# Performance work log

Hardware: AMD Instinct MI355X
Metric: run time of the kernel (lower is better)

The kernel has to match this reference:

```python
import jax, jax.numpy as jnp
import numpy as np
import math

B, S, D, K = 8, 2048, 1024, 64
EPS = 1e-5

def _ln(x):
    m = jnp.mean(x, axis=-1, keepdims=True)
    v = jnp.mean((x - m) ** 2, axis=-1, keepdims=True)
    return (x - m) * jax.lax.rsqrt(v + EPS)

def setup_inputs() -> dict:
    key = jax.random.key(0)
    ks = jax.random.split(key, 14)
    s = 0.02
    return {
        "x":  jax.random.normal(ks[0], (B, S, D), dtype=jnp.float32),
        "Wk": jax.random.normal(ks[1], (D, K), dtype=jnp.float32) * s,
        "bk": jnp.zeros((K,), dtype=jnp.float32),
        "Wq": jax.random.normal(ks[2], (D, K), dtype=jnp.float32) * s,
        "bq": jnp.zeros((K,), dtype=jnp.float32),
        "Wv": jax.random.normal(ks[3], (D, D), dtype=jnp.float32) * s,
        "bv": jnp.zeros((D,), dtype=jnp.float32),
        "Wb": jax.random.normal(ks[4], (D, 1), dtype=jnp.float32) * s,
        "bb": jnp.zeros((1,), dtype=jnp.float32),
        "W1": jax.random.normal(ks[5], (D, D), dtype=jnp.float32) * s,
        "b1": jnp.zeros((D,), dtype=jnp.float32),
        "g1": jnp.ones((D,), dtype=jnp.float32),
        "be1": jnp.zeros((D,), dtype=jnp.float32),
    }

def reference(x, Wk, bk, Wq, bq, Wv, bv, Wb, bb, W1, b1, g1, be1):
    scale = 1.0 / math.sqrt(K)
    keys    = (jnp.einsum('bsd,dk->bsk', x, Wk) + bk) * scale   # [B,S,K]
    queries = jnp.einsum('bsd,dk->bsk', x, Wq) + bq             # [B,S,K]
    values  = jnp.einsum('bsd,de->bse', x, Wv) + bv             # [B,S,D]
    biases  = jnp.einsum('bsd,do->bso', x, Wb) + bb             # [B,S,1]
    # scores[b,i,j] = keys[b,i] . queries[b,j] + biases[b,i]
    scores = jax.nn.sigmoid(jnp.einsum('bik,bjk->bij', keys, queries) + biases)
    attention = jnp.einsum('bij,bjd->bid', scores, values)      # [B,S,D]
    res = _ln(x + attention) * g1 + be1
    feedforward = jax.nn.relu(jnp.einsum('bsd,de->bse', res, W1) + b1)
    return _ln(res + feedforward)
```

## Files before the change

### kernel.cpp

```cpp
#include <hip/hip_runtime.h>
#include <math.h>


typedef __bf16 bf16_t;
typedef __bf16 bf16x4_t __attribute__((ext_vector_type(4)));
typedef __bf16 bf16x8_t __attribute__((ext_vector_type(8)));
typedef float  f32x4    __attribute__((ext_vector_type(4)));

#define DEV static __device__ __forceinline__

DEV void gll16(const void* g, void* l) {
  __builtin_amdgcn_global_load_lds(
      (const __attribute__((address_space(1))) void*)g,
      (__attribute__((address_space(3))) void*)l, 16, 0, 0);
}

template <int MODE, int MFAST>
__global__ __launch_bounds__(512, 2) void gemm256p(
    const bf16_t* __restrict__ A, const bf16_t* __restrict__ B,
    bf16_t* __restrict__ C, int K, int lda, int ldb, int ldc,
    long sAb, long sBb, long sCb, const float* __restrict__ aux0) {
  const int gx = gridDim.x, gy = gridDim.y;
  const int gxy = gx * gy;
  const int nwg = gxy * (int)gridDim.z;
  const int orig = blockIdx.x + gx * blockIdx.y + gxy * blockIdx.z;
  const int lid = (orig & 7) * (nwg >> 3) + (orig >> 3);
  const int bz = lid / gxy;
  const int rem = lid - bz * gxy;
  const int bx = MFAST ? (rem / gy) : (rem % gx);
  const int by = MFAST ? (rem % gy) : (rem / gx);

  A += (long)bz * sAb;
  B += (long)bz * sBb;
  const int m0 = by * 256, n0 = bx * 256;

  __shared__ bf16_t SM[65536];
#define ASH(b, h) (&SM[(((b)*2 + (h)) << 13)])
#define BSH(b, h) (&SM[32768 + (((b)*2 + (h)) << 13)])

  const int tid = threadIdx.x;
  const int wid = tid >> 6, l = tid & 63;
  const int wr = wid >> 2, wc = wid & 3;
  const int lr = l & 15, lh = l >> 4;

  const int sRow = tid >> 2;
  const int sSl = (tid & 3) ^ ((tid >> 3) & 3);
  const bf16_t* Asrc = A + (long)(m0 + sRow) * lda + sSl * 8;
  const bf16_t* Bsrc = B + (long)(n0 + sRow) * ldb + sSl * 8;
  const long aStep = (long)128 * lda, bStep = (long)128 * ldb;

#define STAGE_A(b, h, kt) do { \
    const bf16_t* s_ = Asrc + (kt) * 64 + (h) * 32; \
    gll16(s_,         ASH(b, h) + tid * 8); \
    gll16(s_ + aStep, ASH(b, h) + 4096 + tid * 8); } while (0)
#define STAGE_B(b, h, kt) do { \
    const bf16_t* s_ = Bsrc + (kt) * 64 + (h) * 32; \
    gll16(s_,         BSH(b, h) + tid * 8); \
    gll16(s_ + bStep, BSH(b, h) + 4096 + tid * 8); } while (0)

  const int sw = (lh ^ ((lr >> 1) & 3)) * 8;
  const int aOff = (wr * 128 + lr) * 32 + sw;
  const int bOff = (wc * 64 + lr) * 32 + sw;

  f32x4 acc[8][4] = {};
  const int NT = K >> 6;

#define LGKM(n) do { \
    asm volatile("s_waitcnt lgkmcnt(" #n ")" ::: "memory"); \
    __builtin_amdgcn_sched_barrier(0); } while (0)
#define MFMA16(AS, BS, mo) do { \
    __builtin_amdgcn_s_setprio(1); \
    _Pragma("unroll") for (int m = 0; m < 4; ++m) \
    _Pragma("unroll") for (int n = 0; n < 4; ++n) \
      acc[m + (mo)][n] = __builtin_amdgcn_mfma_f32_16x16x32_bf16(AS[m], BS[n], acc[m + (mo)][n], 0, 0, 0); \
    __builtin_amdgcn_s_setprio(0); } while (0)

  STAGE_A(0, 0, 0); STAGE_B(0, 0, 0); STAGE_A(0, 1, 0); STAGE_B(0, 1, 0);
  asm volatile("s_waitcnt vmcnt(4)" ::: "memory");
  __builtin_amdgcn_s_barrier();

  bf16x8_t aA[4], aB[4], bA[4], bB[4];
#pragma unroll
  for (int n = 0; n < 4; ++n) bA[n] = *(const bf16x8_t*)(BSH(0, 0) + bOff + n * 512);
#pragma unroll
  for (int m = 0; m < 4; ++m) aA[m] = *(const bf16x8_t*)(ASH(0, 0) + aOff + m * 512);

  for (int t = 0; t < NT; ++t) {
    const int p = t & 1, q = p ^ 1;
    const bool pf = (t + 1 < NT);

#pragma unroll
    for (int m = 0; m < 4; ++m) aB[m] = *(const bf16x8_t*)(ASH(p, 0) + aOff + (m + 4) * 512);
    if (pf) STAGE_A(q, 0, t + 1);
    LGKM(4);
    MFMA16(aA, bA, 0);

    if (pf) {
      asm volatile("s_waitcnt vmcnt(2)" ::: "memory");
    } else {
      asm volatile("s_waitcnt vmcnt(0)" ::: "memory");
    }
    __builtin_amdgcn_sched_barrier(0);
    __builtin_amdgcn_s_barrier();
#pragma unroll
    for (int m = 0; m < 4; ++m) aA[m] = *(const bf16x8_t*)(ASH(p, 1) + aOff + m * 512);
#pragma unroll
    for (int n = 0; n < 4; ++n) bB[n] = *(const bf16x8_t*)(BSH(p, 1) + bOff + n * 512);
    if (pf) STAGE_B(q, 0, t + 1);
    LGKM(8);
    MFMA16(aB, bA, 4);

#pragma unroll
    for (int m = 0; m < 4; ++m) aB[m] = *(const bf16x8_t*)(ASH(p, 1) + aOff + (m + 4) * 512);
    if (pf) STAGE_A(q, 1, t + 1);
    LGKM(4);
    MFMA16(aA, bB, 0);

    if (pf) STAGE_B(q, 1, t + 1);
    asm volatile("s_waitcnt lgkmcnt(0)" ::: "memory");
    if (pf) {
      asm volatile("s_waitcnt vmcnt(4)" ::: "memory");
    }
    __builtin_amdgcn_sched_barrier(0);
    __builtin_amdgcn_s_barrier();
    if (pf) {
#pragma unroll
      for (int n = 0; n < 4; ++n) bA[n] = *(const bf16x8_t*)(BSH(q, 0) + bOff + n * 512);
#pragma unroll
      for (int m = 0; m < 4; ++m) aA[m] = *(const bf16x8_t*)(ASH(q, 0) + aOff + m * 512);
    }
    __builtin_amdgcn_sched_barrier(0);
    MFMA16(aB, bB, 4);
  }
#undef STAGE_A
#undef STAGE_B
#undef LGKM
#undef MFMA16

  bf16_t* Cb = C + (long)bz * sCb;
  const int rowb = m0 + wr * 128 + lh * 4;
  const int colb = n0 + wc * 64 + lr;
#pragma unroll
  for (int m = 0; m < 8; ++m)
#pragma unroll
    for (int n = 0; n < 4; ++n) {
      const f32x4 v = acc[m][n];
      const int cc = colb + n * 16;
#pragma unroll
      for (int r = 0; r < 4; ++r) {
        const int rr = rowb + m * 16 + r;
        const float val = v[r];
        if constexpr (MODE == 1) {
          Cb[(long)rr * ldc + cc] = (bf16_t)(val + aux0[rr]);
        } else if constexpr (MODE == 3) {
          Cb[(long)rr * ldc + cc] = (bf16_t)val;
        } else {
          Cb[(long)rr * ldc + cc] = (bf16_t)fmaxf(val + aux0[cc], 0.0f);
        }
      }
    }
#undef ASH
#undef BSH
}

__global__ __launch_bounds__(256) void scores128(
    const bf16_t* __restrict__ kq, bf16_t* __restrict__ C,
    const float* __restrict__ biases) {
  const int orig = blockIdx.x + 16 * blockIdx.y + 256 * blockIdx.z;
  const int lid = (orig & 7) * 256 + (orig >> 3);
  const int bz = lid >> 8;
  const int rem = lid & 255;
  const int bx = rem & 15, by = rem >> 4;

  const bf16_t* A = kq + (long)bz * 2048 * 128;
  const bf16_t* B = A + 64;
  const float* a0 = biases + (long)bz * 2048;
  const int m0 = by * 128, n0 = bx * 128;

  __shared__ bf16_t SM[16384];
#define ASH(h) (&SM[(h) << 12])
#define BSH(h) (&SM[8192 + ((h) << 12)])

  const int tid = threadIdx.x;
  const int w = tid >> 6, l = tid & 63;
  const int wr = w >> 1, wc = w & 1;
  const int lr = l & 15, lh = l >> 4;

  const int sRow = tid >> 2;
  const int sSl = ((tid & 3) ^ ((tid >> 3) & 3)) * 8;
  const bf16_t* As = A + (long)(m0 + sRow) * 128 + sSl;
  const bf16_t* Bs = B + (long)(n0 + sRow) * 128 + sSl;
#pragma unroll
  for (int h = 0; h < 2; ++h) {
    gll16(As + h * 32, ASH(h) + tid * 8);
    gll16(As + h * 32 + 64 * 128, ASH(h) + 2048 + tid * 8);
    gll16(Bs + h * 32, BSH(h) + tid * 8);
    gll16(Bs + h * 32 + 64 * 128, BSH(h) + 2048 + tid * 8);
  }
  asm volatile("s_waitcnt vmcnt(0)" ::: "memory");
  __builtin_amdgcn_s_barrier();

  const int sw = (lh ^ ((lr >> 1) & 3)) * 8;
  const int aOff = (wr * 64 + lr) * 32 + sw;
  const int bOff = (wc * 64 + lr) * 32 + sw;

  f32x4 acc[4][4] = {};
#pragma unroll
  for (int h = 0; h < 2; ++h) {
    bf16x8_t aF[4], bF[4];
#pragma unroll
    for (int m = 0; m < 4; ++m) aF[m] = *(const bf16x8_t*)(ASH(h) + aOff + m * 512);
#pragma unroll
    for (int n = 0; n < 4; ++n) bF[n] = *(const bf16x8_t*)(BSH(h) + bOff + n * 512);
#pragma unroll
    for (int m = 0; m < 4; ++m)
#pragma unroll
      for (int n = 0; n < 4; ++n)
        acc[m][n] = __builtin_amdgcn_mfma_f32_16x16x32_bf16(aF[m], bF[n], acc[m][n], 0, 0, 0);
  }

  __builtin_amdgcn_s_barrier();
  {
    const int rowb = (wr << 6) + (lh << 2);
    const int colb = (wc << 6) + lr;
#pragma unroll
    for (int m = 0; m < 4; ++m)
#pragma unroll
      for (int n = 0; n < 4; ++n) {
        const f32x4 v = acc[m][n];
        const int cl = colb + (n << 4);
#pragma unroll
        for (int r = 0; r < 4; ++r) {
          const int rl = rowb + (m << 4) + r;
          const float zz = v[r] + a0[m0 + rl];
          SM[rl * 128 + (cl ^ (lh << 4))] =
              (bf16_t)__builtin_amdgcn_rcpf(1.0f + __expf(-zz));
        }
      }
    __syncthreads();
    bf16_t* Cb = C + (long)bz * 2048 * 2048;
    const int chunk = tid & 15, rsub = tid >> 4;
#pragma unroll
    for (int pp = 0; pp < 8; ++pp) {
      const int rl = pp * 16 + rsub;
      const int sc = chunk ^ (((rl >> 2) & 3) << 1);
      const bf16x8_t vv = *(const bf16x8_t*)&SM[rl * 128 + sc * 8];
      *(bf16x8_t*)&Cb[(long)(m0 + rl) * 2048 + n0 + chunk * 8] = vv;
    }
  }
#undef ASH
#undef BSH
}

__global__ __launch_bounds__(256) void kq_thin(
    const bf16_t* __restrict__ A, const bf16_t* __restrict__ B,
    bf16_t* __restrict__ C,
    const float* __restrict__ bk, const float* __restrict__ bq) {
  const int m0 = blockIdx.x * 64;

  __shared__ bf16_t SM[12288];
#define ASH(b) (&SM[(b) << 11])
#define BSH(b) (&SM[4096 + ((b) << 12)])

  const int tid = threadIdx.x;
  const int w = tid >> 6, l = tid & 63;
  const int lr = l & 15, lh = l >> 4;

  const int sRow = tid >> 2;
  const int sSl = (tid & 3) ^ ((tid >> 3) & 3);
  const bf16_t* Asrc = A + (long)(m0 + sRow) * 1024 + sSl * 8;
  const bf16_t* Bsrc0 = B + (long)sRow * 1024 + sSl * 8;
  const bf16_t* Bsrc1 = B + (long)(64 + sRow) * 1024 + sSl * 8;

  const int sw = (lh ^ ((lr >> 1) & 3)) * 8;
  const int aOff = (w * 16 + lr) * 32 + sw;

  f32x4 acc[8] = {};

  auto stage = [&](int buf, int k0) {
    gll16(Asrc + k0, ASH(buf) + tid * 8);
    gll16(Bsrc0 + k0, BSH(buf) + tid * 8);
    gll16(Bsrc1 + k0, BSH(buf) + 2048 + tid * 8);
  };

  stage(0, 0);
  __syncthreads();
  int cur = 0;

  for (int k0 = 0; k0 < 1024; k0 += 32) {
    if (k0 + 32 < 1024) stage(cur ^ 1, k0 + 32);

    const bf16x8_t aF = *(const bf16x8_t*)(ASH(cur) + aOff);
    bf16x8_t bF[8];
#pragma unroll
    for (int j = 0; j < 8; ++j)
      bF[j] = *(const bf16x8_t*)(BSH(cur) + (j * 16 + lr) * 32 + sw);
#pragma unroll
    for (int j = 0; j < 8; ++j)
      acc[j] = __builtin_amdgcn_mfma_f32_16x16x32_bf16(aF, bF[j], acc[j], 0, 0, 0);

    __syncthreads();
    cur ^= 1;
  }

  {
#pragma unroll
    for (int j = 0; j < 8; ++j) {
      const f32x4 v = acc[j];
      const int cl = j * 16 + lr;
      const float b = (cl < 64) ? bk[cl] : bq[cl - 64];
      const float s = (cl < 64) ? 0.125f : 1.0f;
#pragma unroll
      for (int r = 0; r < 4; ++r) {
        const int rl = w * 16 + lh * 4 + r;
        SM[rl * 128 + (cl ^ (lh << 4))] = (bf16_t)((v[r] + b) * s);
      }
    }
    __syncthreads();
    const int chunk = tid & 15, rsub = tid >> 4;
#pragma unroll
    for (int pp = 0; pp < 4; ++pp) {
      const int rl = pp * 16 + rsub;
      const int sc = chunk ^ (((rl >> 2) & 3) << 1);
      const bf16x8_t vv = *(const bf16x8_t*)&SM[rl * 128 + sc * 8];
      *(bf16x8_t*)&C[(long)(m0 + rl) * 128 + chunk * 8] = vv;
    }
  }
#undef ASH
#undef BSH
}

__global__ __launch_bounds__(256) void cast_bias_kernel(
    const float* __restrict__ x, const float* __restrict__ Wb,
    const float* __restrict__ bb, bf16_t* __restrict__ x_bf,
    float* __restrict__ biases) {
  const int r = blockIdx.x * 4 + (threadIdx.x >> 6);
  const int l = threadIdx.x & 63;
  const float* xr = x + (long)r * 1024;
  bf16_t* orow = x_bf + (long)r * 1024;
  float s = 0.f;
#pragma unroll
  for (int i = 0; i < 4; ++i) {
    const int off = l * 4 + i * 256;
    const float4 v = *(const float4*)(xr + off);
    const float4 w = *(const float4*)(Wb + off);
    s += v.x * w.x + v.y * w.y + v.z * w.z + v.w * w.w;
    bf16x4_t o;
    o[0] = (bf16_t)v.x; o[1] = (bf16_t)v.y; o[2] = (bf16_t)v.z; o[3] = (bf16_t)v.w;
    *(bf16x4_t*)(orow + off) = o;
  }
#pragma unroll
  for (int off = 1; off < 64; off <<= 1) s += __shfl_xor(s, off);
  if (l == 0) biases[r] = s + bb[0];
}

__global__ __launch_bounds__(256) void transpose_cast_kernel(
    const float* __restrict__ in, bf16_t* __restrict__ out, int R, int C) {
  __shared__ float t[32][33];
  const int c0 = blockIdx.x * 32, r0 = blockIdx.y * 32;
  const int tx = threadIdx.x & 31, ty = threadIdx.x >> 5;
#pragma unroll
  for (int i = 0; i < 4; ++i) {
    const int rl = ty * 4 + i;
    t[rl][tx] = in[(long)(r0 + rl) * C + c0 + tx];
  }
  __syncthreads();
#pragma unroll
  for (int i = 0; i < 4; ++i) {
    const int rl = ty * 4 + i;
    out[(long)(c0 + rl) * R + r0 + tx] = (bf16_t)t[tx][rl];
  }
}

__global__ __launch_bounds__(256) void ln1_kernel(
    const bf16_t* __restrict__ x, const bf16_t* __restrict__ attn,
    const float* __restrict__ g, const float* __restrict__ be,
    bf16_t* __restrict__ res) {
  const int w = threadIdx.x >> 6, l = threadIdx.x & 63;
  const long r = (long)blockIdx.x * 4 + w;
  const bf16_t* xr = x + r * 1024;
  const bf16_t* ar = attn + r * 1024;
  float y[16];
  float s = 0.f, ss = 0.f;
#pragma unroll
  for (int h = 0; h < 2; ++h) {
    const int base = h * 512 + l * 8;
    const bf16x8_t xv = *(const bf16x8_t*)(xr + base);
    const bf16x8_t av = *(const bf16x8_t*)(ar + base);
#pragma unroll
    for (int j = 0; j < 8; ++j) {
      const float yy = (float)xv[j] + (float)av[j];
      y[h * 8 + j] = yy;
      s += yy; ss += yy * yy;
    }
  }
#pragma unroll
  for (int off = 1; off < 64; off <<= 1) {
    s += __shfl_xor(s, off);
    ss += __shfl_xor(ss, off);
  }
  const float mean = s * (1.0f / 1024.0f);
  const float rs = rsqrtf(ss * (1.0f / 1024.0f) - mean * mean + 1e-5f);
  bf16_t* orow = res + r * 1024;
#pragma unroll
  for (int h = 0; h < 2; ++h) {
    const int base = h * 512 + l * 8;
    bf16x8_t o;
#pragma unroll
    for (int j = 0; j < 8; ++j)
      o[j] = (bf16_t)((y[h * 8 + j] - mean) * rs * g[base + j] + be[base + j]);
    *(bf16x8_t*)(orow + base) = o;
  }
}

__global__ __launch_bounds__(256) void ln2_kernel(
    const bf16_t* __restrict__ res, const bf16_t* __restrict__ hh,
    float* __restrict__ out) {
  const int w = threadIdx.x >> 6, l = threadIdx.x & 63;
  const long r = (long)blockIdx.x * 4 + w;
  const bf16_t* rr = res + r * 1024;
  const bf16_t* hr = hh + r * 1024;
  float y[16];
  float s = 0.f, ss = 0.f;
#pragma unroll
  for (int h = 0; h < 2; ++h) {
    const int base = h * 512 + l * 8;
    const bf16x8_t rv = *(const bf16x8_t*)(rr + base);
    const bf16x8_t hv = *(const bf16x8_t*)(hr + base);
#pragma unroll
    for (int j = 0; j < 8; ++j) {
      const float yy = (float)rv[j] + (float)hv[j];
      y[h * 8 + j] = yy;
      s += yy; ss += yy * yy;
    }
  }
#pragma unroll
  for (int off = 1; off < 64; off <<= 1) {
    s += __shfl_xor(s, off);
    ss += __shfl_xor(ss, off);
  }
  const float mean = s * (1.0f / 1024.0f);
  const float rs = rsqrtf(ss * (1.0f / 1024.0f) - mean * mean + 1e-5f);
  float* orow = out + r * 1024;
#pragma unroll
  for (int h = 0; h < 2; ++h) {
    const int base = h * 512 + l * 8;
    float4 o1, o2;
    o1.x = (y[h * 8 + 0] - mean) * rs; o1.y = (y[h * 8 + 1] - mean) * rs;
    o1.z = (y[h * 8 + 2] - mean) * rs; o1.w = (y[h * 8 + 3] - mean) * rs;
    o2.x = (y[h * 8 + 4] - mean) * rs; o2.y = (y[h * 8 + 5] - mean) * rs;
    o2.z = (y[h * 8 + 6] - mean) * rs; o2.w = (y[h * 8 + 7] - mean) * rs;
    *(float4*)(orow + base) = o1;
    *(float4*)(orow + base + 4) = o2;
  }
}

extern "C" void kernel_launch(void* const* d_in, const int* in_sizes, int n_in,
                              void* d_out, int out_size, void* d_ws, size_t ws_size,
                              hipStream_t stream) {
  const float* x   = (const float*)d_in[0];
  const float* Wk  = (const float*)d_in[1];
  const float* bk  = (const float*)d_in[2];
  const float* Wq  = (const float*)d_in[3];
  const float* bq  = (const float*)d_in[4];
  const float* Wv  = (const float*)d_in[5];
  const float* bv  = (const float*)d_in[6];
  const float* Wb  = (const float*)d_in[7];
  const float* bb  = (const float*)d_in[8];
  const float* W1  = (const float*)d_in[9];
  const float* b1  = (const float*)d_in[10];
  const float* g1  = (const float*)d_in[11];
  const float* be1 = (const float*)d_in[12];
  float* out = (float*)d_out;

  char* ws = (char*)d_ws;
  bf16_t* x_bf    = (bf16_t*)(ws + 0);
  bf16_t* vt_bf   = (bf16_t*)(ws + 33554432);
  bf16_t* kq_bf   = (bf16_t*)(ws + 67108864);
  bf16_t* Wkqt    = (bf16_t*)(ws + 71303168);
  bf16_t* Wvt     = (bf16_t*)(ws + 71565312);
  bf16_t* W1t     = (bf16_t*)(ws + 73662464);
  float*  biases  = (float*) (ws + 75759616);
  bf16_t* scores  = (bf16_t*)(ws + 75825152);
  bf16_t* attn_bf = (bf16_t*)(ws + 142934016);
  bf16_t* res_bf  = (bf16_t*)(ws + 176488448);
  bf16_t* h_bf    = attn_bf;

  cast_bias_kernel<<<4096, 256, 0, stream>>>(x, Wb, bb, x_bf, biases);
  transpose_cast_kernel<<<dim3(2, 32), 256, 0, stream>>>(Wk, Wkqt, 1024, 64);
  transpose_cast_kernel<<<dim3(2, 32), 256, 0, stream>>>(Wq, Wkqt + 64 * 1024, 1024, 64);
  transpose_cast_kernel<<<dim3(32, 32), 256, 0, stream>>>(Wv, Wvt, 1024, 1024);
  transpose_cast_kernel<<<dim3(32, 32), 256, 0, stream>>>(W1, W1t, 1024, 1024);

  kq_thin<<<256, 256, 0, stream>>>(x_bf, Wkqt, kq_bf, bk, bq);

  gemm256p<1, 1><<<dim3(64, 4, 1), 512, 0, stream>>>(
      Wvt, x_bf, vt_bf, 1024, 1024, 1024, 16384, 0, 0, 0, bv);

  scores128<<<dim3(16, 16, 8), 256, 0, stream>>>(kq_bf, scores, biases);

  gemm256p<3, 0><<<dim3(4, 8, 8), 512, 0, stream>>>(
      scores, vt_bf, attn_bf, 2048, 2048, 16384, 1024,
      2048L * 2048, 2048, 2048L * 1024, nullptr);

  ln1_kernel<<<4096, 256, 0, stream>>>(x_bf, attn_bf, g1, be1, res_bf);

  gemm256p<4, 0><<<dim3(4, 64, 1), 512, 0, stream>>>(
      res_bf, W1t, h_bf, 1024, 1024, 1024, 1024, 0, 0, 0, b1);

  ln2_kernel<<<4096, 256, 0, stream>>>(res_bf, h_bf, out);
}
```

Measured before the change: 237.6 us.

## Add 256x128-tile GEMM for V and FFN projections; merge weight transposes

Adds a new GEMM kernel with 256x128 tiles, a smaller LDS footprint and occupancy target 4. It is used for the value projection and the FFN GEMM, which doubles the block count for these 1024-wide-K GEMMs so more CUs stay busy. The four weight transpose-cast launches are also merged into a single launch to cut launch overhead. The cost is less data reuse per tile and a simpler pipeline than the 256x256 kernel.

```diff
diff --git a/kernel.cpp b/kernel.cpp
--- a/kernel.cpp
+++ b/kernel.cpp
@@ -16,6 +16,96 @@
 }
 
 template <int MODE, int MFAST>
+__global__ __launch_bounds__(512, 4) void gemm128n(
+    const bf16_t* __restrict__ A, const bf16_t* __restrict__ B,
+    bf16_t* __restrict__ C, int K, int lda, int ldb, int ldc,
+    const float* __restrict__ aux0) {
+  const int gx = gridDim.x, gy = gridDim.y;
+  const int nwg = gx * gy;
+  const int orig = blockIdx.x + gx * blockIdx.y;
+  const int lid = (orig & 7) * (nwg >> 3) + (orig >> 3);
+  const int bx = MFAST ? (lid / gy) : (lid % gx);
+  const int by = MFAST ? (lid % gy) : (lid / gx);
+  const int m0 = by * 256, n0 = bx * 128;
+
+  __shared__ bf16_t SM[24576];
+#define ASH(s) (&SM[(s) << 13])
+#define BSH(s) (&SM[16384 + ((s) << 12)])
+
+  const int tid = threadIdx.x;
+  const int wid = tid >> 6, l = tid & 63;
+  const int wr = wid >> 1, wc = wid & 1;
+  const int lr = l & 15, lh = l >> 4;
+
+  const int sRow = tid >> 2;
+  const int sSl = (tid & 3) ^ ((tid >> 3) & 3);
+  const bf16_t* Asrc = A + (long)(m0 + sRow) * lda + sSl * 8;
+  const bf16_t* Bsrc = B + (long)(n0 + sRow) * ldb + sSl * 8;
+  const long aStep = (long)128 * lda;
+
+  const int sw = (lh ^ ((lr >> 1) & 3)) * 8;
+  const int aOff = (wr * 64 + lr) * 32 + sw;
+  const int bOff = (wc * 64 + lr) * 32 + sw;
+
+  f32x4 acc[4][4] = {};
+  const int NT = K >> 5;
+
+  gll16(Asrc, ASH(0) + tid * 8);
+  gll16(Asrc + aStep, ASH(0) + 4096 + tid * 8);
+  gll16(Bsrc, BSH(0) + tid * 8);
+
+  for (int h = 0; h < NT; ++h) {
+    const int s = h & 1;
+    asm volatile("s_waitcnt vmcnt(0)" ::: "memory");
+    __builtin_amdgcn_sched_barrier(0);
+    __builtin_amdgcn_s_barrier();
+    if (h + 1 < NT) {
+      const bf16_t* a_ = Asrc + (h + 1) * 32;
+      const bf16_t* b_ = Bsrc + (h + 1) * 32;
+      gll16(a_, ASH(s ^ 1) + tid * 8);
+      gll16(a_ + aStep, ASH(s ^ 1) + 4096 + tid * 8);
+      gll16(b_, BSH(s ^ 1) + tid * 8);
+    }
+    bf16x8_t aF[4], bF[4];
+#pragma unroll
+    for (int m = 0; m < 4; ++m) aF[m] = *(const bf16x8_t*)(ASH(s) + aOff + m * 512);
+#pragma unroll
+    for (int n = 0; n < 4; ++n) bF[n] = *(const bf16x8_t*)(BSH(s) + bOff + n * 512);
+    asm volatile("s_waitcnt lgkmcnt(0)" ::: "memory");
+    __builtin_amdgcn_sched_barrier(0);
+    __builtin_amdgcn_s_setprio(1);
+#pragma unroll
+    for (int m = 0; m < 4; ++m)
+#pragma unroll
+      for (int n = 0; n < 4; ++n)
+        acc[m][n] = __builtin_amdgcn_mfma_f32_16x16x32_bf16(aF[m], bF[n], acc[m][n], 0, 0, 0);
+    __builtin_amdgcn_s_setprio(0);
+  }
+
+  const int rowb = m0 + wr * 64 + lh * 4;
+  const int colb = n0 + wc * 64 + lr;
+#pragma unroll
+  for (int m = 0; m < 4; ++m)
+#pragma unroll
+    for (int n = 0; n < 4; ++n) {
+      const f32x4 v = acc[m][n];
+      const int cc = colb + n * 16;
+#pragma unroll
+      for (int r = 0; r < 4; ++r) {
+        const int rr = rowb + m * 16 + r;
+        const float val = v[r];
+        if constexpr (MODE == 1) {
+          C[(long)rr * ldc + cc] = (bf16_t)(val + aux0[rr]);
+        } else {
+          C[(long)rr * ldc + cc] = (bf16_t)fmaxf(val + aux0[cc], 0.0f);
+        }
+      }
+    }
+#undef ASH
+#undef BSH
+}
+
+template <int MODE>
 __global__ __launch_bounds__(512, 2) void gemm256p(
     const bf16_t* __restrict__ A, const bf16_t* __restrict__ B,
     bf16_t* __restrict__ C, int K, int lda, int ldb, int ldc,
@@ -27,8 +117,8 @@
   const int lid = (orig & 7) * (nwg >> 3) + (orig >> 3);
   const int bz = lid / gxy;
   const int rem = lid - bz * gxy;
-  const int bx = MFAST ? (rem / gy) : (rem % gx);
-  const int by = MFAST ? (rem % gy) : (rem / gx);
+  const int bx = rem % gx;
+  const int by = rem / gx;
 
   A += (long)bz * sAb;
   B += (long)bz * sBb;
@@ -149,14 +239,7 @@
 #pragma unroll
       for (int r = 0; r < 4; ++r) {
         const int rr = rowb + m * 16 + r;
-        const float val = v[r];
-        if constexpr (MODE == 1) {
-          Cb[(long)rr * ldc + cc] = (bf16_t)(val + aux0[rr]);
-        } else if constexpr (MODE == 3) {
-          Cb[(long)rr * ldc + cc] = (bf16_t)val;
-        } else {
-          Cb[(long)rr * ldc + cc] = (bf16_t)fmaxf(val + aux0[cc], 0.0f);
-        }
+        Cb[(long)rr * ldc + cc] = (bf16_t)v[r];
       }
     }
 #undef ASH
@@ -354,10 +437,29 @@
   if (l == 0) biases[r] = s + bb[0];
 }
 
-__global__ __launch_bounds__(256) void transpose_cast_kernel(
-    const float* __restrict__ in, bf16_t* __restrict__ out, int R, int C) {
+__global__ __launch_bounds__(256) void transpose_all(
+    const float* __restrict__ Wk, const float* __restrict__ Wq,
+    const float* __restrict__ Wv, const float* __restrict__ W1,
+    bf16_t* __restrict__ Wkqt, bf16_t* __restrict__ Wvt,
+    bf16_t* __restrict__ W1t) {
+  int b = blockIdx.x;
+  const float* in;
+  bf16_t* out;
+  int R, C, c0, r0;
+  if (b < 1024) {
+    in = Wv; out = Wvt; R = 1024; C = 1024;
+    c0 = (b & 31) * 32; r0 = (b >> 5) * 32;
+  } else if (b < 2048) {
+    b -= 1024; in = W1; out = W1t; R = 1024; C = 1024;
+    c0 = (b & 31) * 32; r0 = (b >> 5) * 32;
+  } else if (b < 2112) {
+    b -= 2048; in = Wk; out = Wkqt; R = 1024; C = 64;
+    c0 = (b & 1) * 32; r0 = (b >> 1) * 32;
+  } else {
+    b -= 2112; in = Wq; out = Wkqt + 64 * 1024; R = 1024; C = 64;
+    c0 = (b & 1) * 32; r0 = (b >> 1) * 32;
+  }
   __shared__ float t[32][33];
-  const int c0 = blockIdx.x * 32, r0 = blockIdx.y * 32;
   const int tx = threadIdx.x & 31, ty = threadIdx.x >> 5;
 #pragma unroll
   for (int i = 0; i < 4; ++i) {
@@ -487,26 +589,23 @@
   bf16_t* h_bf    = attn_bf;
 
   cast_bias_kernel<<<4096, 256, 0, stream>>>(x, Wb, bb, x_bf, biases);
-  transpose_cast_kernel<<<dim3(2, 32), 256, 0, stream>>>(Wk, Wkqt, 1024, 64);
-  transpose_cast_kernel<<<dim3(2, 32), 256, 0, stream>>>(Wq, Wkqt + 64 * 1024, 1024, 64);
-  transpose_cast_kernel<<<dim3(32, 32), 256, 0, stream>>>(Wv, Wvt, 1024, 1024);
-  transpose_cast_kernel<<<dim3(32, 32), 256, 0, stream>>>(W1, W1t, 1024, 1024);
+  transpose_all<<<2176, 256, 0, stream>>>(Wk, Wq, Wv, W1, Wkqt, Wvt, W1t);
 
   kq_thin<<<256, 256, 0, stream>>>(x_bf, Wkqt, kq_bf, bk, bq);
 
-  gemm256p<1, 1><<<dim3(64, 4, 1), 512, 0, stream>>>(
-      Wvt, x_bf, vt_bf, 1024, 1024, 1024, 16384, 0, 0, 0, bv);
+  gemm128n<1, 1><<<dim3(128, 4), 512, 0, stream>>>(
+      Wvt, x_bf, vt_bf, 1024, 1024, 1024, 16384, bv);
 
   scores128<<<dim3(16, 16, 8), 256, 0, stream>>>(kq_bf, scores, biases);
 
-  gemm256p<3, 0><<<dim3(4, 8, 8), 512, 0, stream>>>(
+  gemm256p<3><<<dim3(4, 8, 8), 512, 0, stream>>>(
       scores, vt_bf, attn_bf, 2048, 2048, 16384, 1024,
       2048L * 2048, 2048, 2048L * 1024, nullptr);
 
   ln1_kernel<<<4096, 256, 0, stream>>>(x_bf, attn_bf, g1, be1, res_bf);
 
-  gemm256p<4, 0><<<dim3(4, 64, 1), 512, 0, stream>>>(
-      res_bf, W1t, h_bf, 1024, 1024, 1024, 1024, 0, 0, 0, b1);
+  gemm128n<4, 0><<<dim3(8, 64), 512, 0, stream>>>(
+      res_bf, W1t, h_bf, 1024, 1024, 1024, 1024, b1);
 
   ln2_kernel<<<4096, 256, 0, stream>>>(res_bf, h_bf, out);
 }
```

Result: no change. 235.5 us (-0.9%).
